# Optimization experiments

Measured on AMD Instinct MI355X. Metric: run time of the kernel, lower is better.

The kernel has to match this reference:

```python
import jax, jax.numpy as jnp
import numpy as np
import math

B, T, C = 4, 2048, 1024
N_HEADS = 16
D_HEAD = C // N_HEADS


def _rope_tables(d_head, max_seq_len):
    half = d_head // 2
    theta = 1.0 / (10000.0 ** (jnp.arange(half, dtype=jnp.float32) / half))
    pos = jnp.arange(max_seq_len, dtype=jnp.float32)
    freqs = jnp.outer(pos, theta)  # [S, half]
    cos = jnp.concatenate([jnp.cos(freqs), jnp.cos(freqs)], axis=-1)  # [S, d_head]
    sin = jnp.concatenate([jnp.sin(freqs), jnp.sin(freqs)], axis=-1)
    return cos, sin


def _rotate_half(x):
    d = x.shape[-1] // 2
    return jnp.concatenate([-x[..., d:], x[..., :d]], axis=-1)


def _apply_rope(x, cos, sin):
    # x: [B, H, T, d_head]; cos/sin: [T, d_head] broadcast over B,H
    return x * cos[None, None] + _rotate_half(x) * sin[None, None]


def setup_inputs() -> dict:
    key = jax.random.key(0)
    k1, k2, k3 = jax.random.split(key, 3)
    x = jax.random.normal(k1, (B, T, C), dtype=jnp.float32)
    W_qkv = jax.random.normal(k2, (C, 3 * C), dtype=jnp.float32) * (1.0 / math.sqrt(C))
    W_proj = jax.random.normal(k3, (C, C), dtype=jnp.float32) * (1.0 / math.sqrt(C))
    return {"x": x, "W_qkv": W_qkv, "W_proj": W_proj}


def reference(x, W_qkv, W_proj):
    b, t, c = x.shape
    qkv = x @ W_qkv  # [B, T, 3C]
    q, k, v = jnp.split(qkv, 3, axis=-1)

    def reshape(z):
        return z.reshape(b, t, N_HEADS, D_HEAD).transpose(0, 2, 1, 3)  # [B,H,T,dh]

    q, k, v = reshape(q), reshape(k), reshape(v)

    cos, sin = _rope_tables(D_HEAD, t)
    q = _apply_rope(q, cos, sin)
    k = _apply_rope(k, cos, sin)

    scale = 1.0 / math.sqrt(D_HEAD)
    att = jnp.einsum('bhqd,bhkd->bhqk', q, k) * scale  # [B,H,T,T]
    causal = jnp.tril(jnp.ones((t, t), dtype=bool))
    att = jnp.where(causal[None, None], att, -jnp.inf)
    att = jax.nn.softmax(att, axis=-1)
    out = jnp.einsum('bhqk,bhkd->bhqd', att, v)  # [B,H,T,dh]
    out = out.transpose(0, 2, 1, 3).reshape(b, t, c)
    return out @ W_proj
```

## Files before the change

kernel.cpp:

```cpp
#include <hip/hip_runtime.h>
#include <stdint.h>

#define Bz 4
#define Tz 2048
#define Cz 1024
#define NHz 16
#define DHz 64
#define Mz (Bz*Tz)

typedef unsigned short u16;
typedef __attribute__((ext_vector_type(8))) short short8;
typedef __attribute__((ext_vector_type(8))) unsigned short ushort8v;
typedef __attribute__((ext_vector_type(4))) unsigned short u16x4;
typedef __attribute__((ext_vector_type(4))) float f32x4;
typedef __attribute__((ext_vector_type(2))) unsigned int uint2v;

__device__ __forceinline__ float bf2f(u16 u){
  union { unsigned int i; float f; } v; v.i = ((unsigned int)u) << 16; return v.f;
}
__device__ __forceinline__ u16 f2bf(float f){
  union { float f; unsigned int i; } v; v.f = f;
  unsigned int r = v.i + 0x7FFFu + ((v.i >> 16) & 1u);
  return (u16)(r >> 16);
}


__global__ void k_cast_bf16(const float* __restrict__ in, u16* __restrict__ out, int n4){
  int i = blockIdx.x*256 + threadIdx.x;
  if (i >= n4) return;
  float4 v = ((const float4*)in)[i];
  u16x4 o;
  o[0] = f2bf(v.x); o[1] = f2bf(v.y); o[2] = f2bf(v.z); o[3] = f2bf(v.w);
  *(u16x4*)(out + (size_t)i*4) = o;
}

__global__ void k_transpose_cast(const float* __restrict__ W, u16* __restrict__ Wt, int K, int N){
  __shared__ float tile[32][33];
  int n0 = blockIdx.x*32, k0 = blockIdx.y*32;
  int tx = threadIdx.x, ty = threadIdx.y;
  #pragma unroll
  for (int i = 0; i < 32; i += 8)
    tile[ty+i][tx] = W[(size_t)(k0+ty+i)*N + n0 + tx];
  __syncthreads();
  #pragma unroll
  for (int i = 0; i < 32; i += 8)
    Wt[(size_t)(n0+ty+i)*K + k0 + tx] = f2bf(tile[tx][ty+i]);
}

__global__ void k_rope_tables(float* __restrict__ cosT, float* __restrict__ sinT){
  int idx = blockIdx.x*256 + threadIdx.x;
  int t = idx >> 5, i = idx & 31;
  float theta = exp2f(-(float)i * (13.287712379549449f / 32.0f));
  float ang = (float)t * theta;
  cosT[idx] = cosf(ang);
  sinT[idx] = sinf(ang);
}

#define GLDS(src, dstE) __builtin_amdgcn_global_load_lds( \
    (const __attribute__((address_space(1))) unsigned int*)(src), \
    (__attribute__((address_space(3))) unsigned int*)(lds + (dstE)), 16, 0, 0)

template<int Nn, int Kk, bool OUT_BF16, bool ROPE>
__global__ __launch_bounds__(512, 2) void k_gemm8(const u16* __restrict__ A, const u16* __restrict__ Bt,
                       void* __restrict__ Cout, u16* __restrict__ vTout,
                       const float* __restrict__ cosT, const float* __restrict__ sinT){
  extern __shared__ u16 lds[];
  constexpr int NT = Kk/64;
  constexpr int BUFE = 24576;
  constexpr int NWG = (Mz/128)*(Nn/256);
  const int wg = (blockIdx.x & 7)*(NWG/8) + (blockIdx.x >> 3);
  const int bm = wg & 63, bn = wg >> 6;
  const int tid = threadIdx.x, lane = tid & 63, w = tid >> 6;
  const int wm = w >> 2, wn = w & 3;
  const int g = lane >> 4, r = lane & 15;

  const int srow8 = lane >> 3;
  const int sslot = (lane & 7) ^ srow8;
  const u16* asrc = A  + (size_t)(bm*128 + w*16 + srow8)*Kk + sslot*8;
  const u16* bsrc = Bt + (size_t)(bn*256 + w*16 + srow8)*Kk + sslot*8;
  const int dA  = w*1024 + lane*8;
  const int dB0 = 8192 + w*1024 + lane*8;
  const int dB1 = 16384 + w*1024 + lane*8;

  int a_off[2][2][2], b_off[2][2][2];
  #pragma unroll
  for (int rq = 0; rq < 2; ++rq)
    #pragma unroll
    for (int fi = 0; fi < 2; ++fi)
      #pragma unroll
      for (int kc = 0; kc < 2; ++kc){
        int row = wm*64 + rq*32 + fi*16 + r;
        a_off[rq][fi][kc] = (row*128 + kc*64 + g*16) ^ ((r & 7) << 4);
        int rowb = wn*64 + rq*32 + fi*16 + r;
        b_off[rq][fi][kc] = 16384 + ((rowb*128 + kc*64 + g*16) ^ ((r & 7) << 4));
      }

  f32x4 acc[4][4] = {};

  {
    GLDS(asrc,                     dA);        GLDS(asrc + 8*(size_t)Kk,                     dA + 512);
    GLDS(bsrc,                     dB0);       GLDS(bsrc + 8*(size_t)Kk,                     dB0 + 512);
    GLDS(bsrc + 128*(size_t)Kk,    dB1);       GLDS(bsrc + 136*(size_t)Kk,                   dB1 + 512);
    GLDS(asrc + 64,                BUFE + dA); GLDS(asrc + 64 + 8*(size_t)Kk,                BUFE + dA + 512);
    GLDS(bsrc + 64,                BUFE + dB0);GLDS(bsrc + 64 + 8*(size_t)Kk,                BUFE + dB0 + 512);
    GLDS(bsrc + 64 + 128*(size_t)Kk, BUFE + dB1); GLDS(bsrc + 64 + 136*(size_t)Kk,           BUFE + dB1 + 512);
  }

  int bufc = 0;
  #pragma unroll 1
  for (int t = 0; t < NT; ++t){
    if (t + 1 < NT) asm volatile("s_waitcnt vmcnt(6)" ::: "memory");
    else            asm volatile("s_waitcnt vmcnt(0)" ::: "memory");
    __builtin_amdgcn_s_barrier();

    const int cbB = bufc*(BUFE*2);
    const bool pre = (t + 2 < NT);
    int bufn = bufc + 2; if (bufn >= 3) bufn -= 3;
    const int nE = bufn*BUFE;
    const size_t ko = (size_t)(t+2)*64;

    #define LD8(off) (*(const short8*)((const char*)lds + (off)))
    short8 af0k0, af0k1, af1k0, af1k1;
    short8 b0f0k0, b0f0k1, b0f1k0, b0f1k1;
    short8 b1f0k0, b1f0k1, b1f1k0, b1f1k1;

    af0k0 = LD8(cbB + a_off[0][0][0]); af0k1 = LD8(cbB + a_off[0][0][1]);
    af1k0 = LD8(cbB + a_off[0][1][0]); af1k1 = LD8(cbB + a_off[0][1][1]);
    b0f0k0 = LD8(cbB + b_off[0][0][0]); b0f0k1 = LD8(cbB + b_off[0][0][1]);
    b0f1k0 = LD8(cbB + b_off[0][1][0]); b0f1k1 = LD8(cbB + b_off[0][1][1]);
    if (pre){ GLDS(asrc + ko, nE + dA); GLDS(asrc + ko + 8*(size_t)Kk, nE + dA + 512); }
    __builtin_amdgcn_s_setprio(1);
    acc[0][0] = __builtin_amdgcn_mfma_f32_16x16x32_bf16(af0k0, b0f0k0, acc[0][0], 0,0,0);
    acc[0][0] = __builtin_amdgcn_mfma_f32_16x16x32_bf16(af0k1, b0f0k1, acc[0][0], 0,0,0);
    acc[0][1] = __builtin_amdgcn_mfma_f32_16x16x32_bf16(af0k0, b0f1k0, acc[0][1], 0,0,0);
    acc[0][1] = __builtin_amdgcn_mfma_f32_16x16x32_bf16(af0k1, b0f1k1, acc[0][1], 0,0,0);
    acc[1][0] = __builtin_amdgcn_mfma_f32_16x16x32_bf16(af1k0, b0f0k0, acc[1][0], 0,0,0);
    acc[1][0] = __builtin_amdgcn_mfma_f32_16x16x32_bf16(af1k1, b0f0k1, acc[1][0], 0,0,0);
    acc[1][1] = __builtin_amdgcn_mfma_f32_16x16x32_bf16(af1k0, b0f1k0, acc[1][1], 0,0,0);
    acc[1][1] = __builtin_amdgcn_mfma_f32_16x16x32_bf16(af1k1, b0f1k1, acc[1][1], 0,0,0);
    __builtin_amdgcn_s_setprio(0);

    b1f0k0 = LD8(cbB + b_off[1][0][0]); b1f0k1 = LD8(cbB + b_off[1][0][1]);
    b1f1k0 = LD8(cbB + b_off[1][1][0]); b1f1k1 = LD8(cbB + b_off[1][1][1]);
    if (pre){ GLDS(bsrc + ko, nE + dB0); GLDS(bsrc + ko + 8*(size_t)Kk, nE + dB0 + 512); }
    __builtin_amdgcn_s_setprio(1);
    acc[0][2] = __builtin_amdgcn_mfma_f32_16x16x32_bf16(af0k0, b1f0k0, acc[0][2], 0,0,0);
    acc[0][2] = __builtin_amdgcn_mfma_f32_16x16x32_bf16(af0k1, b1f0k1, acc[0][2], 0,0,0);
    acc[0][3] = __builtin_amdgcn_mfma_f32_16x16x32_bf16(af0k0, b1f1k0, acc[0][3], 0,0,0);
    acc[0][3] = __builtin_amdgcn_mfma_f32_16x16x32_bf16(af0k1, b1f1k1, acc[0][3], 0,0,0);
    acc[1][2] = __builtin_amdgcn_mfma_f32_16x16x32_bf16(af1k0, b1f0k0, acc[1][2], 0,0,0);
    acc[1][2] = __builtin_amdgcn_mfma_f32_16x16x32_bf16(af1k1, b1f0k1, acc[1][2], 0,0,0);
    acc[1][3] = __builtin_amdgcn_mfma_f32_16x16x32_bf16(af1k0, b1f1k0, acc[1][3], 0,0,0);
    acc[1][3] = __builtin_amdgcn_mfma_f32_16x16x32_bf16(af1k1, b1f1k1, acc[1][3], 0,0,0);
    __builtin_amdgcn_s_setprio(0);

    af0k0 = LD8(cbB + a_off[1][0][0]); af0k1 = LD8(cbB + a_off[1][0][1]);
    af1k0 = LD8(cbB + a_off[1][1][0]); af1k1 = LD8(cbB + a_off[1][1][1]);
    if (pre){ GLDS(bsrc + ko + 128*(size_t)Kk, nE + dB1); GLDS(bsrc + ko + 136*(size_t)Kk, nE + dB1 + 512); }
    __builtin_amdgcn_s_setprio(1);
    acc[2][2] = __builtin_amdgcn_mfma_f32_16x16x32_bf16(af0k0, b1f0k0, acc[2][2], 0,0,0);
    acc[2][2] = __builtin_amdgcn_mfma_f32_16x16x32_bf16(af0k1, b1f0k1, acc[2][2], 0,0,0);
    acc[2][3] = __builtin_amdgcn_mfma_f32_16x16x32_bf16(af0k0, b1f1k0, acc[2][3], 0,0,0);
    acc[2][3] = __builtin_amdgcn_mfma_f32_16x16x32_bf16(af0k1, b1f1k1, acc[2][3], 0,0,0);
    acc[3][2] = __builtin_amdgcn_mfma_f32_16x16x32_bf16(af1k0, b1f0k0, acc[3][2], 0,0,0);
    acc[3][2] = __builtin_amdgcn_mfma_f32_16x16x32_bf16(af1k1, b1f0k1, acc[3][2], 0,0,0);
    acc[3][3] = __builtin_amdgcn_mfma_f32_16x16x32_bf16(af1k0, b1f1k0, acc[3][3], 0,0,0);
    acc[3][3] = __builtin_amdgcn_mfma_f32_16x16x32_bf16(af1k1, b1f1k1, acc[3][3], 0,0,0);
    __builtin_amdgcn_s_setprio(0);

    __builtin_amdgcn_s_setprio(1);
    acc[2][0] = __builtin_amdgcn_mfma_f32_16x16x32_bf16(af0k0, b0f0k0, acc[2][0], 0,0,0);
    acc[2][0] = __builtin_amdgcn_mfma_f32_16x16x32_bf16(af0k1, b0f0k1, acc[2][0], 0,0,0);
    acc[2][1] = __builtin_amdgcn_mfma_f32_16x16x32_bf16(af0k0, b0f1k0, acc[2][1], 0,0,0);
    acc[2][1] = __builtin_amdgcn_mfma_f32_16x16x32_bf16(af0k1, b0f1k1, acc[2][1], 0,0,0);
    acc[3][0] = __builtin_amdgcn_mfma_f32_16x16x32_bf16(af1k0, b0f0k0, acc[3][0], 0,0,0);
    acc[3][0] = __builtin_amdgcn_mfma_f32_16x16x32_bf16(af1k1, b0f0k1, acc[3][0], 0,0,0);
    acc[3][1] = __builtin_amdgcn_mfma_f32_16x16x32_bf16(af1k0, b0f1k0, acc[3][1], 0,0,0);
    acc[3][1] = __builtin_amdgcn_mfma_f32_16x16x32_bf16(af1k1, b0f1k1, acc[3][1], 0,0,0);
    __builtin_amdgcn_s_setprio(0);
    #undef LD8

    ++bufc; if (bufc >= 3) bufc = 0;
  }

  const int nbase = bn*256 + wn*64;
  if (ROPE && nbase >= 2048){
    const int b = (bm*128) >> 11;
    const int h = (nbase >> 6) & 15;
    #pragma unroll
    for (int ri = 0; ri < 4; ++ri){
      const int m0 = bm*128 + wm*64 + ri*16 + 4*g;
      const int t0 = m0 & (Tz-1);
      #pragma unroll
      for (int cj = 0; cj < 4; ++cj){
        const int d = cj*16 + r;
        u16x4 o;
        #pragma unroll
        for (int jj = 0; jj < 4; ++jj) o[jj] = f2bf(acc[ri][cj][jj]);
        *(u16x4*)(vTout + ((size_t)((b*16 + h)*64 + d))*2048 + t0) = o;
      }
    }
  } else if (ROPE){
    const float qs = (nbase < 1024) ? 0.18033688011112042f : 1.0f;
    #pragma unroll
    for (int ri = 0; ri < 4; ++ri)
      #pragma unroll
      for (int jj = 0; jj < 4; ++jj){
        const int m = bm*128 + wm*64 + ri*16 + 4*g + jj;
        const int t = m & (Tz-1);
        #pragma unroll
        for (int cj = 0; cj < 2; ++cj){
          const int ch = cj*16 + r;
          float cv = cosT[t*32 + ch];
          float sv = sinT[t*32 + ch];
          float lo = acc[ri][cj][jj], hi = acc[ri][cj+2][jj];
          ((u16*)Cout)[(size_t)m*Nn + nbase + ch]      = f2bf((lo*cv - hi*sv)*qs);
          ((u16*)Cout)[(size_t)m*Nn + nbase + ch + 32] = f2bf((hi*cv + lo*sv)*qs);
        }
      }
  } else {
    #pragma unroll
    for (int ri = 0; ri < 4; ++ri)
      #pragma unroll
      for (int cj = 0; cj < 4; ++cj)
        #pragma unroll
        for (int jj = 0; jj < 4; ++jj){
          const size_t m = bm*128 + wm*64 + ri*16 + 4*g + jj;
          const size_t n = (size_t)nbase + cj*16 + r;
          if (OUT_BF16) ((u16*)Cout)[m*Nn + n] = f2bf(acc[ri][cj][jj]);
          else          ((float*)Cout)[m*Nn + n] = acc[ri][cj][jj];
        }
  }
}

__global__ __launch_bounds__(512) void k_attn2(const u16* __restrict__ qkv,
                                               const u16* __restrict__ vT,
                                               u16* __restrict__ att){
  __shared__ u16 K_lds[2*4096];
  __shared__ u16 V_lds[2*4096];
  __shared__ u16 P_lds[8*16*72];

  const int bh = blockIdx.x;
  const int b = bh >> 4, h = bh & 15;
  const int tid = threadIdx.x;
  const int w = tid >> 6;
  const int lane = tid & 63;
  const int g = lane >> 4;
  const int ql = lane & 15;
  u16* Pw = P_lds + w*16*72;

  const int srow  = lane >> 3;
  const int sslot = (lane & 7) ^ srow;
  const u16* ksrc = qkv + ((size_t)(b*Tz + 8*w + srow))*3072 + 1024 + h*64 + sslot*8;
  const u16* vsrc = vT  + ((size_t)bh*64 + 8*w + srow)*2048 + sslot*8;
  u16* kdst = K_lds + w*512 + lane*8;
  u16* vdst = V_lds + w*512 + lane*8;

  short8 ones;
  #pragma unroll
  for (int i = 0; i < 8; ++i) ones[i] = (short)0x3F80;

  int fofs[4][2];
  #pragma unroll
  for (int t = 0; t < 4; ++t){
    int row = 16*t + ql;
    fofs[t][0] = (row*128 + 16*g)      ^ ((row & 7) << 4);
    fofs[t][1] = (row*128 + 64 + 16*g) ^ ((row & 7) << 4);
  }

  #pragma unroll 1
  for (int half = 0; half < 2; ++half){
    const int qt = (half == 0) ? blockIdx.y : (15 - blockIdx.y);
    const int qr0w = qt*128 + w*16;
    const int nt = 2*qt + 2;

    const u16* qsrc = qkv + (size_t)(b*Tz + qr0w + ql)*3072 + h*64;
    short8 qf0 = *(const short8*)(qsrc + g*8);
    short8 qf1 = *(const short8*)(qsrc + 32 + g*8);

    f32x4 acc[4] = {{0,0,0,0},{0,0,0,0},{0,0,0,0},{0,0,0,0}};
    f32x4 accl = {0,0,0,0};

    __builtin_amdgcn_global_load_lds(
      (const __attribute__((address_space(1))) unsigned int*)(ksrc),
      (__attribute__((address_space(3))) unsigned int*)(kdst), 16, 0, 0);
    __builtin_amdgcn_global_load_lds(
      (const __attribute__((address_space(1))) unsigned int*)(vsrc),
      (__attribute__((address_space(3))) unsigned int*)(vdst), 16, 0, 0);
    __syncthreads();

    #pragma unroll 2
    for (int kt = 0; kt < nt; ++kt){
      const int buf = kt & 1;
      if (kt + 1 < nt){
        __builtin_amdgcn_global_load_lds(
          (const __attribute__((address_space(1))) unsigned int*)(ksrc + (size_t)(kt+1)*64*3072),
          (__attribute__((address_space(3))) unsigned int*)(kdst + (buf^1)*4096), 16, 0, 0);
        __builtin_amdgcn_global_load_lds(
          (const __attribute__((address_space(1))) unsigned int*)(vsrc + (kt+1)*64),
          (__attribute__((address_space(3))) unsigned int*)(vdst + (buf^1)*4096), 16, 0, 0);
      }
      const char* Kb = (const char*)(K_lds + buf*4096);
      const char* Vb = (const char*)(V_lds + buf*4096);
      const int kv0 = kt*64;

      f32x4 st[4];
      __builtin_amdgcn_s_setprio(1);
      #pragma unroll
      for (int t = 0; t < 4; ++t){
        short8 kf0 = *(const short8*)(Kb + fofs[t][0]);
        short8 kf1 = *(const short8*)(Kb + fofs[t][1]);
        f32x4 z = {0,0,0,0};
        z = __builtin_amdgcn_mfma_f32_16x16x32_bf16(kf0, qf0, z, 0, 0, 0);
        z = __builtin_amdgcn_mfma_f32_16x16x32_bf16(kf1, qf1, z, 0, 0, 0);
        st[t] = z;
      }
      __builtin_amdgcn_s_setprio(0);

      if (kv0 + 63 > qr0w){
        const int qg = qr0w + ql;
        #pragma unroll
        for (int t = 0; t < 4; ++t)
          #pragma unroll
          for (int j = 0; j < 4; ++j)
            if (kv0 + 16*t + 4*g + j > qg) st[t][j] = -1e30f;
      }

      #pragma unroll
      for (int t = 0; t < 4; ++t){
        float p0, p1, p2, p3;
        asm("v_exp_f32 %0, %1" : "=v"(p0) : "v"(st[t][0]));
        asm("v_exp_f32 %0, %1" : "=v"(p1) : "v"(st[t][1]));
        asm("v_exp_f32 %0, %1" : "=v"(p2) : "v"(st[t][2]));
        asm("v_exp_f32 %0, %1" : "=v"(p3) : "v"(st[t][3]));
        unsigned int lov, hiv;
        asm("v_cvt_pk_bf16_f32 %0, %1, %2" : "=v"(lov) : "v"(p0), "v"(p1));
        asm("v_cvt_pk_bf16_f32 %0, %1, %2" : "=v"(hiv) : "v"(p2), "v"(p3));
        uint2v pv; pv[0] = lov; pv[1] = hiv;
        *(uint2v*)((char*)Pw + ql*144 + (16*t + 4*g)*2) = pv;
      }

      short8 pf0 = *(const short8*)((char*)Pw + ql*144 + 16*g);
      short8 pf1 = *(const short8*)((char*)Pw + ql*144 + 64 + 16*g);
      __builtin_amdgcn_s_setprio(1);
      accl = __builtin_amdgcn_mfma_f32_16x16x32_bf16(pf0, ones, accl, 0, 0, 0);
      accl = __builtin_amdgcn_mfma_f32_16x16x32_bf16(pf1, ones, accl, 0, 0, 0);
      #pragma unroll
      for (int dt = 0; dt < 4; ++dt){
        short8 vf0 = *(const short8*)(Vb + fofs[dt][0]);
        short8 vf1 = *(const short8*)(Vb + fofs[dt][1]);
        acc[dt] = __builtin_amdgcn_mfma_f32_16x16x32_bf16(pf0, vf0, acc[dt], 0, 0, 0);
        acc[dt] = __builtin_amdgcn_mfma_f32_16x16x32_bf16(pf1, vf1, acc[dt], 0, 0, 0);
      }
      __builtin_amdgcn_s_setprio(0);
      __syncthreads();
    }

    float lj[4];
    #pragma unroll
    for (int j = 0; j < 4; ++j) lj[j] = 1.0f / accl[j];
    #pragma unroll
    for (int dt = 0; dt < 4; ++dt)
      #pragma unroll
      for (int j = 0; j < 4; ++j)
        att[(size_t)(b*Tz + qr0w + 4*g + j)*Cz + h*64 + dt*16 + ql] = f2bf(acc[dt][j]*lj[j]);
  }
}


extern "C" void kernel_launch(void* const* d_in, const int* in_sizes, int n_in,
                              void* d_out, int out_size, void* d_ws, size_t ws_size,
                              hipStream_t stream){
  const float* x     = (const float*)d_in[0];
  const float* Wqkv  = (const float*)d_in[1];
  const float* Wproj = (const float*)d_in[2];
  float* out = (float*)d_out;
  char* ws = (char*)d_ws;

  u16*  xb   = (u16*)(ws);
  u16*  wqt  = (u16*)(ws + 16777216);
  u16*  wpt  = (u16*)(ws + 23068672);
  u16*  qkv  = (u16*)(ws + 25165824);
  u16*  vTr  = (u16*)(ws + 75497472);
  float* cosT = (float*)(ws + 92274688);
  float* sinT = (float*)(ws + 92536832);

  hipFuncSetAttribute(reinterpret_cast<const void*>(k_gemm8<3072,1024,true,true>),
                      hipFuncAttributeMaxDynamicSharedMemorySize, 147456);
  hipFuncSetAttribute(reinterpret_cast<const void*>(k_gemm8<1024,1024,false,false>),
                      hipFuncAttributeMaxDynamicSharedMemorySize, 147456);

  k_cast_bf16<<<Mz*Cz/4/256, 256, 0, stream>>>(x, xb, Mz*Cz/4);
  k_transpose_cast<<<dim3(3072/32, 1024/32), dim3(32,8), 0, stream>>>(Wqkv, wqt, 1024, 3072);
  k_transpose_cast<<<dim3(1024/32, 1024/32), dim3(32,8), 0, stream>>>(Wproj, wpt, 1024, 1024);
  k_rope_tables<<<Tz*32/256, 256, 0, stream>>>(cosT, sinT);

  k_gemm8<3072, 1024, true, true><<<(Mz/128)*(3072/256), 512, 147456, stream>>>(
      xb, wqt, qkv, vTr, cosT, sinT);
  k_attn2<<<dim3(Bz*NHz, 8), 512, 0, stream>>>(qkv, vTr, xb);
  k_gemm8<1024, 1024, false, false><<<(Mz/128)*(1024/256), 512, 147456, stream>>>(
      xb, wpt, out, nullptr, nullptr, nullptr);
}
```

Measured before the change: 161.5 us.

## Restructure GEMM main loop into two barrier-synchronized phases with hoisted A fragments

Reorganizes the QKV GEMM inner loop into two phases. All A fragments and the first half of the B fragments are loaded up front, and 16 MFMAs run per phase, with the global-to-LDS prefetches split 3/3 across the phases. The vmcnt wait and barrier move from the top of the iteration to the end, with a prologue wait added before the loop. Extra s_barriers and explicit lgkmcnt(0) waits are inserted so the waves stay in lockstep, ping-pong style. The aim is better overlap of LDS reads, global prefetch and MFMA issue. The cost is more barriers per iteration and higher register pressure from holding all A fragments at once.

```diff
diff --git a/kernel.cpp b/kernel.cpp
--- a/kernel.cpp
+++ b/kernel.cpp
@@ -105,14 +105,12 @@
     GLDS(bsrc + 64,                BUFE + dB0);GLDS(bsrc + 64 + 8*(size_t)Kk,                BUFE + dB0 + 512);
     GLDS(bsrc + 64 + 128*(size_t)Kk, BUFE + dB1); GLDS(bsrc + 64 + 136*(size_t)Kk,           BUFE + dB1 + 512);
   }
+  asm volatile("s_waitcnt vmcnt(6)" ::: "memory");
+  __builtin_amdgcn_s_barrier();
 
   int bufc = 0;
   #pragma unroll 1
   for (int t = 0; t < NT; ++t){
-    if (t + 1 < NT) asm volatile("s_waitcnt vmcnt(6)" ::: "memory");
-    else            asm volatile("s_waitcnt vmcnt(0)" ::: "memory");
-    __builtin_amdgcn_s_barrier();
-
     const int cbB = bufc*(BUFE*2);
     const bool pre = (t + 2 < NT);
     int bufn = bufc + 2; if (bufn >= 3) bufn -= 3;
@@ -120,64 +118,70 @@
     const size_t ko = (size_t)(t+2)*64;
 
     #define LD8(off) (*(const short8*)((const char*)lds + (off)))
-    short8 af0k0, af0k1, af1k0, af1k1;
-    short8 b0f0k0, b0f0k1, b0f1k0, b0f1k1;
-    short8 b1f0k0, b1f0k1, b1f1k0, b1f1k1;
-
-    af0k0 = LD8(cbB + a_off[0][0][0]); af0k1 = LD8(cbB + a_off[0][0][1]);
-    af1k0 = LD8(cbB + a_off[0][1][0]); af1k1 = LD8(cbB + a_off[0][1][1]);
-    b0f0k0 = LD8(cbB + b_off[0][0][0]); b0f0k1 = LD8(cbB + b_off[0][0][1]);
-    b0f1k0 = LD8(cbB + b_off[0][1][0]); b0f1k1 = LD8(cbB + b_off[0][1][1]);
-    if (pre){ GLDS(asrc + ko, nE + dA); GLDS(asrc + ko + 8*(size_t)Kk, nE + dA + 512); }
+
+    short8 a0k0 = LD8(cbB + a_off[0][0][0]), a0k1 = LD8(cbB + a_off[0][0][1]);
+    short8 a1k0 = LD8(cbB + a_off[0][1][0]), a1k1 = LD8(cbB + a_off[0][1][1]);
+    short8 a2k0 = LD8(cbB + a_off[1][0][0]), a2k1 = LD8(cbB + a_off[1][0][1]);
+    short8 a3k0 = LD8(cbB + a_off[1][1][0]), a3k1 = LD8(cbB + a_off[1][1][1]);
+    short8 b0k0 = LD8(cbB + b_off[0][0][0]), b0k1 = LD8(cbB + b_off[0][0][1]);
+    short8 b1k0 = LD8(cbB + b_off[0][1][0]), b1k1 = LD8(cbB + b_off[0][1][1]);
+    if (pre){
+      GLDS(asrc + ko,                 nE + dA);
+      GLDS(asrc + ko + 8*(size_t)Kk,  nE + dA + 512);
+      GLDS(bsrc + ko,                 nE + dB0);
+    }
+    __builtin_amdgcn_s_barrier();
+    asm volatile("s_waitcnt lgkmcnt(0)" ::: "memory");
     __builtin_amdgcn_s_setprio(1);
-    acc[0][0] = __builtin_amdgcn_mfma_f32_16x16x32_bf16(af0k0, b0f0k0, acc[0][0], 0,0,0);
-    acc[0][0] = __builtin_amdgcn_mfma_f32_16x16x32_bf16(af0k1, b0f0k1, acc[0][0], 0,0,0);
-    acc[0][1] = __builtin_amdgcn_mfma_f32_16x16x32_bf16(af0k0, b0f1k0, acc[0][1], 0,0,0);
-    acc[0][1] = __builtin_amdgcn_mfma_f32_16x16x32_bf16(af0k1, b0f1k1, acc[0][1], 0,0,0);
-    acc[1][0] = __builtin_amdgcn_mfma_f32_16x16x32_bf16(af1k0, b0f0k0, acc[1][0], 0,0,0);
-    acc[1][0] = __builtin_amdgcn_mfma_f32_16x16x32_bf16(af1k1, b0f0k1, acc[1][0], 0,0,0);
-    acc[1][1] = __builtin_amdgcn_mfma_f32_16x16x32_bf16(af1k0, b0f1k0, acc[1][1], 0,0,0);
-    acc[1][1] = __builtin_amdgcn_mfma_f32_16x16x32_bf16(af1k1, b0f1k1, acc[1][1], 0,0,0);
+    acc[0][0] = __builtin_amdgcn_mfma_f32_16x16x32_bf16(a0k0, b0k0, acc[0][0], 0,0,0);
+    acc[0][0] = __builtin_amdgcn_mfma_f32_16x16x32_bf16(a0k1, b0k1, acc[0][0], 0,0,0);
+    acc[0][1] = __builtin_amdgcn_mfma_f32_16x16x32_bf16(a0k0, b1k0, acc[0][1], 0,0,0);
+    acc[0][1] = __builtin_amdgcn_mfma_f32_16x16x32_bf16(a0k1, b1k1, acc[0][1], 0,0,0);
+    acc[1][0] = __builtin_amdgcn_mfma_f32_16x16x32_bf16(a1k0, b0k0, acc[1][0], 0,0,0);
+    acc[1][0] = __builtin_amdgcn_mfma_f32_16x16x32_bf16(a1k1, b0k1, acc[1][0], 0,0,0);
+    acc[1][1] = __builtin_amdgcn_mfma_f32_16x16x32_bf16(a1k0, b1k0, acc[1][1], 0,0,0);
+    acc[1][1] = __builtin_amdgcn_mfma_f32_16x16x32_bf16(a1k1, b1k1, acc[1][1], 0,0,0);
+    acc[2][0] = __builtin_amdgcn_mfma_f32_16x16x32_bf16(a2k0, b0k0, acc[2][0], 0,0,0);
+    acc[2][0] = __builtin_amdgcn_mfma_f32_16x16x32_bf16(a2k1, b0k1, acc[2][0], 0,0,0);
+    acc[2][1] = __builtin_amdgcn_mfma_f32_16x16x32_bf16(a2k0, b1k0, acc[2][1], 0,0,0);
+    acc[2][1] = __builtin_amdgcn_mfma_f32_16x16x32_bf16(a2k1, b1k1, acc[2][1], 0,0,0);
+    acc[3][0] = __builtin_amdgcn_mfma_f32_16x16x32_bf16(a3k0, b0k0, acc[3][0], 0,0,0);
+    acc[3][0] = __builtin_amdgcn_mfma_f32_16x16x32_bf16(a3k1, b0k1, acc[3][0], 0,0,0);
+    acc[3][1] = __builtin_amdgcn_mfma_f32_16x16x32_bf16(a3k0, b1k0, acc[3][1], 0,0,0);
+    acc[3][1] = __builtin_amdgcn_mfma_f32_16x16x32_bf16(a3k1, b1k1, acc[3][1], 0,0,0);
     __builtin_amdgcn_s_setprio(0);
-
-    b1f0k0 = LD8(cbB + b_off[1][0][0]); b1f0k1 = LD8(cbB + b_off[1][0][1]);
-    b1f1k0 = LD8(cbB + b_off[1][1][0]); b1f1k1 = LD8(cbB + b_off[1][1][1]);
-    if (pre){ GLDS(bsrc + ko, nE + dB0); GLDS(bsrc + ko + 8*(size_t)Kk, nE + dB0 + 512); }
+    __builtin_amdgcn_s_barrier();
+
+    short8 c0k0 = LD8(cbB + b_off[1][0][0]), c0k1 = LD8(cbB + b_off[1][0][1]);
+    short8 c1k0 = LD8(cbB + b_off[1][1][0]), c1k1 = LD8(cbB + b_off[1][1][1]);
+    if (pre){
+      GLDS(bsrc + ko + 8*(size_t)Kk,   nE + dB0 + 512);
+      GLDS(bsrc + ko + 128*(size_t)Kk, nE + dB1);
+      GLDS(bsrc + ko + 136*(size_t)Kk, nE + dB1 + 512);
+    }
+    __builtin_amdgcn_s_barrier();
+    asm volatile("s_waitcnt lgkmcnt(0)" ::: "memory");
     __builtin_amdgcn_s_setprio(1);
-    acc[0][2] = __builtin_amdgcn_mfma_f32_16x16x32_bf16(af0k0, b1f0k0, acc[0][2], 0,0,0);
-    acc[0][2] = __builtin_amdgcn_mfma_f32_16x16x32_bf16(af0k1, b1f0k1, acc[0][2], 0,0,0);
-    acc[0][3] = __builtin_amdgcn_mfma_f32_16x16x32_bf16(af0k0, b1f1k0, acc[0][3], 0,0,0);
-    acc[0][3] = __builtin_amdgcn_mfma_f32_16x16x32_bf16(af0k1, b1f1k1, acc[0][3], 0,0,0);
-    acc[1][2] = __builtin_amdgcn_mfma_f32_16x16x32_bf16(af1k0, b1f0k0, acc[1][2], 0,0,0);
-    acc[1][2] = __builtin_amdgcn_mfma_f32_16x16x32_bf16(af1k1, b1f0k1, acc[1][2], 0,0,0);
-    acc[1][3] = __builtin_amdgcn_mfma_f32_16x16x32_bf16(af1k0, b1f1k0, acc[1][3], 0,0,0);
-    acc[1][3] = __builtin_amdgcn_mfma_f32_16x16x32_bf16(af1k1, b1f1k1, acc[1][3], 0,0,0);
+    acc[0][2] = __builtin_amdgcn_mfma_f32_16x16x32_bf16(a0k0, c0k0, acc[0][2], 0,0,0);
+    acc[0][2] = __builtin_amdgcn_mfma_f32_16x16x32_bf16(a0k1, c0k1, acc[0][2], 0,0,0);
+    acc[0][3] = __builtin_amdgcn_mfma_f32_16x16x32_bf16(a0k0, c1k0, acc[0][3], 0,0,0);
+    acc[0][3] = __builtin_amdgcn_mfma_f32_16x16x32_bf16(a0k1, c1k1, acc[0][3], 0,0,0);
+    acc[1][2] = __builtin_amdgcn_mfma_f32_16x16x32_bf16(a1k0, c0k0, acc[1][2], 0,0,0);
+    acc[1][2] = __builtin_amdgcn_mfma_f32_16x16x32_bf16(a1k1, c0k1, acc[1][2], 0,0,0);
+    acc[1][3] = __builtin_amdgcn_mfma_f32_16x16x32_bf16(a1k0, c1k0, acc[1][3], 0,0,0);
+    acc[1][3] = __builtin_amdgcn_mfma_f32_16x16x32_bf16(a1k1, c1k1, acc[1][3], 0,0,0);
+    acc[2][2] = __builtin_amdgcn_mfma_f32_16x16x32_bf16(a2k0, c0k0, acc[2][2], 0,0,0);
+    acc[2][2] = __builtin_amdgcn_mfma_f32_16x16x32_bf16(a2k1, c0k1, acc[2][2], 0,0,0);
+    acc[2][3] = __builtin_amdgcn_mfma_f32_16x16x32_bf16(a2k0, c1k0, acc[2][3], 0,0,0);
+    acc[2][3] = __builtin_amdgcn_mfma_f32_16x16x32_bf16(a2k1, c1k1, acc[2][3], 0,0,0);
+    acc[3][2] = __builtin_amdgcn_mfma_f32_16x16x32_bf16(a3k0, c0k0, acc[3][2], 0,0,0);
+    acc[3][2] = __builtin_amdgcn_mfma_f32_16x16x32_bf16(a3k1, c0k1, acc[3][2], 0,0,0);
+    acc[3][3] = __builtin_amdgcn_mfma_f32_16x16x32_bf16(a3k0, c1k0, acc[3][3], 0,0,0);
+    acc[3][3] = __builtin_amdgcn_mfma_f32_16x16x32_bf16(a3k1, c1k1, acc[3][3], 0,0,0);
     __builtin_amdgcn_s_setprio(0);
-
-    af0k0 = LD8(cbB + a_off[1][0][0]); af0k1 = LD8(cbB + a_off[1][0][1]);
-    af1k0 = LD8(cbB + a_off[1][1][0]); af1k1 = LD8(cbB + a_off[1][1][1]);
-    if (pre){ GLDS(bsrc + ko + 128*(size_t)Kk, nE + dB1); GLDS(bsrc + ko + 136*(size_t)Kk, nE + dB1 + 512); }
-    __builtin_amdgcn_s_setprio(1);
-    acc[2][2] = __builtin_amdgcn_mfma_f32_16x16x32_bf16(af0k0, b1f0k0, acc[2][2], 0,0,0);
-    acc[2][2] = __builtin_amdgcn_mfma_f32_16x16x32_bf16(af0k1, b1f0k1, acc[2][2], 0,0,0);
-    acc[2][3] = __builtin_amdgcn_mfma_f32_16x16x32_bf16(af0k0, b1f1k0, acc[2][3], 0,0,0);
-    acc[2][3] = __builtin_amdgcn_mfma_f32_16x16x32_bf16(af0k1, b1f1k1, acc[2][3], 0,0,0);
-    acc[3][2] = __builtin_amdgcn_mfma_f32_16x16x32_bf16(af1k0, b1f0k0, acc[3][2], 0,0,0);
-    acc[3][2] = __builtin_amdgcn_mfma_f32_16x16x32_bf16(af1k1, b1f0k1, acc[3][2], 0,0,0);
-    acc[3][3] = __builtin_amdgcn_mfma_f32_16x16x32_bf16(af1k0, b1f1k0, acc[3][3], 0,0,0);
-    acc[3][3] = __builtin_amdgcn_mfma_f32_16x16x32_bf16(af1k1, b1f1k1, acc[3][3], 0,0,0);
-    __builtin_amdgcn_s_setprio(0);
-
-    __builtin_amdgcn_s_setprio(1);
-    acc[2][0] = __builtin_amdgcn_mfma_f32_16x16x32_bf16(af0k0, b0f0k0, acc[2][0], 0,0,0);
-    acc[2][0] = __builtin_amdgcn_mfma_f32_16x16x32_bf16(af0k1, b0f0k1, acc[2][0], 0,0,0);
-    acc[2][1] = __builtin_amdgcn_mfma_f32_16x16x32_bf16(af0k0, b0f1k0, acc[2][1], 0,0,0);
-    acc[2][1] = __builtin_amdgcn_mfma_f32_16x16x32_bf16(af0k1, b0f1k1, acc[2][1], 0,0,0);
-    acc[3][0] = __builtin_amdgcn_mfma_f32_16x16x32_bf16(af1k0, b0f0k0, acc[3][0], 0,0,0);
-    acc[3][0] = __builtin_amdgcn_mfma_f32_16x16x32_bf16(af1k1, b0f0k1, acc[3][0], 0,0,0);
-    acc[3][1] = __builtin_amdgcn_mfma_f32_16x16x32_bf16(af1k0, b0f1k0, acc[3][1], 0,0,0);
-    acc[3][1] = __builtin_amdgcn_mfma_f32_16x16x32_bf16(af1k1, b0f1k1, acc[3][1], 0,0,0);
-    __builtin_amdgcn_s_setprio(0);
+    if (t + 2 < NT)      asm volatile("s_waitcnt vmcnt(6)" ::: "memory");
+    else if (t + 1 < NT) asm volatile("s_waitcnt vmcnt(0)" ::: "memory");
+    __builtin_amdgcn_s_barrier();
     #undef LD8
 
     ++bufc; if (bufc >= 3) bufc = 0;
```

New measurement: 165.5 us. +2.5%, slower.

## Replace QKV GEMM with simple single-buffered 128x128 tile kernel

Applied to the files above, without the earlier changes.

The QKV projection moves from the 8-wave, triple-buffered 128x256 tile kernel to a new 256-thread kernel with 128x128 tiles, K-step 32, and a single LDS buffer with syncs around each step. The RoPE and V-transpose epilogue is carried over unchanged, and the ROPE path is removed from k_gemm8. The smaller tile doubles the workgroup count and uses far less LDS, which may raise occupancy. In exchange it drops the prefetch pipelining, so global-to-LDS latency is exposed on every K step.

```diff
diff --git a/kernel.cpp b/kernel.cpp
--- a/kernel.cpp
+++ b/kernel.cpp
@@ -56,14 +56,117 @@
   sinT[idx] = sinf(ang);
 }
 
+template<int Nn, int Kk, bool ROPE>
+__global__ void k_gemm128(const u16* __restrict__ A, const u16* __restrict__ Bt,
+                          void* __restrict__ Cout, u16* __restrict__ vTout,
+                          const float* __restrict__ cosT, const float* __restrict__ sinT){
+  __shared__ u16 Asub[128*32];
+  __shared__ u16 Bsub[128*32];
+  constexpr int NWG = (Mz/128)*(Nn/128);
+  const int wg = (blockIdx.x & 7)*(NWG/8) + (blockIdx.x >> 3);
+  const int bm = wg & 63, bn = wg >> 6;
+  const int tid = threadIdx.x, lane = tid & 63, w = tid >> 6;
+  const int g = lane >> 4, r = lane & 15;
+  const int wm = (w >> 1)*64, wn = (w & 1)*64;
+  f32x4 acc[4][4] = {};
+
+  const int srow4 = lane >> 2;
+  const int sslot = (lane & 3) ^ (srow4 & 3);
+  const u16* arow = A  + (size_t)(bm*128)*Kk;
+  const u16* brow = Bt + (size_t)(bn*128)*Kk;
+
+  int a_ofs[4], b_ofs[4];
+  #pragma unroll
+  for (int i = 0; i < 4; ++i){
+    a_ofs[i] = (wm + i*16 + r)*64 + (((g ^ (r & 3)) & 3) << 4);
+    b_ofs[i] = (wn + i*16 + r)*64 + (((g ^ (r & 3)) & 3) << 4);
+  }
+
+  for (int k0 = 0; k0 < Kk; k0 += 32){
+    #pragma unroll
+    for (int ic = 0; ic < 2; ++ic){
+      int ch = w*2 + ic;
+      int row = ch*16 + srow4;
+      __builtin_amdgcn_global_load_lds(
+        (const __attribute__((address_space(1))) unsigned int*)(arow + (size_t)row*Kk + k0 + sslot*8),
+        (__attribute__((address_space(3))) unsigned int*)(Asub + ch*512 + lane*8), 16, 0, 0);
+      __builtin_amdgcn_global_load_lds(
+        (const __attribute__((address_space(1))) unsigned int*)(brow + (size_t)row*Kk + k0 + sslot*8),
+        (__attribute__((address_space(3))) unsigned int*)(Bsub + ch*512 + lane*8), 16, 0, 0);
+    }
+    __syncthreads();
+    short8 af[4], bfr[4];
+    #pragma unroll
+    for (int i = 0; i < 4; ++i){
+      af[i]  = *(const short8*)((const char*)Asub + a_ofs[i]);
+      bfr[i] = *(const short8*)((const char*)Bsub + b_ofs[i]);
+    }
+    __builtin_amdgcn_s_setprio(1);
+    #pragma unroll
+    for (int i = 0; i < 4; ++i)
+      #pragma unroll
+      for (int j = 0; j < 4; ++j)
+        acc[i][j] = __builtin_amdgcn_mfma_f32_16x16x32_bf16(af[i], bfr[j], acc[i][j], 0, 0, 0);
+    __builtin_amdgcn_s_setprio(0);
+    __syncthreads();
+  }
+
+  const int nbase = bn*128 + wn;
+  if (ROPE && nbase >= 2048){
+    const int b = bm >> 4;
+    const int h = (nbase >> 6) & 15;
+    #pragma unroll
+    for (int ri = 0; ri < 4; ++ri){
+      const int m0 = bm*128 + wm + ri*16 + 4*g;
+      const int t0 = m0 & (Tz-1);
+      #pragma unroll
+      for (int cj = 0; cj < 4; ++cj){
+        const int d = cj*16 + r;
+        u16x4 o;
+        #pragma unroll
+        for (int jj = 0; jj < 4; ++jj) o[jj] = f2bf(acc[ri][cj][jj]);
+        *(u16x4*)(vTout + ((size_t)((b*16 + h)*64 + d))*2048 + t0) = o;
+      }
+    }
+  } else if (ROPE){
+    const float qs = (nbase < 1024) ? 0.18033688011112042f : 1.0f;
+    #pragma unroll
+    for (int ri = 0; ri < 4; ++ri)
+      #pragma unroll
+      for (int jj = 0; jj < 4; ++jj){
+        const int m = bm*128 + wm + ri*16 + 4*g + jj;
+        const int t = m & (Tz-1);
+        #pragma unroll
+        for (int cj = 0; cj < 2; ++cj){
+          const int ch = cj*16 + r;
+          float cv = cosT[t*32 + ch];
+          float sv = sinT[t*32 + ch];
+          float lo = acc[ri][cj][jj], hi = acc[ri][cj+2][jj];
+          ((u16*)Cout)[(size_t)m*Nn + nbase + ch]      = f2bf((lo*cv - hi*sv)*qs);
+          ((u16*)Cout)[(size_t)m*Nn + nbase + ch + 32] = f2bf((hi*cv + lo*sv)*qs);
+        }
+      }
+  } else {
+    #pragma unroll
+    for (int ri = 0; ri < 4; ++ri)
+      #pragma unroll
+      for (int cj = 0; cj < 4; ++cj)
+        #pragma unroll
+        for (int jj = 0; jj < 4; ++jj){
+          const size_t m = bm*128 + wm + ri*16 + 4*g + jj;
+          const size_t n = (size_t)nbase + cj*16 + r;
+          ((float*)Cout)[m*Nn + n] = acc[ri][cj][jj];
+        }
+  }
+}
+
 #define GLDS(src, dstE) __builtin_amdgcn_global_load_lds( \
     (const __attribute__((address_space(1))) unsigned int*)(src), \
     (__attribute__((address_space(3))) unsigned int*)(lds + (dstE)), 16, 0, 0)
 
-template<int Nn, int Kk, bool OUT_BF16, bool ROPE>
+template<int Nn, int Kk, bool OUT_BF16>
 __global__ __launch_bounds__(512, 2) void k_gemm8(const u16* __restrict__ A, const u16* __restrict__ Bt,
-                       void* __restrict__ Cout, u16* __restrict__ vTout,
-                       const float* __restrict__ cosT, const float* __restrict__ sinT){
+                       void* __restrict__ Cout){
   extern __shared__ u16 lds[];
   constexpr int NT = Kk/64;
   constexpr int BUFE = 24576;
@@ -184,53 +287,17 @@
   }
 
   const int nbase = bn*256 + wn*64;
-  if (ROPE && nbase >= 2048){
-    const int b = (bm*128) >> 11;
-    const int h = (nbase >> 6) & 15;
-    #pragma unroll
-    for (int ri = 0; ri < 4; ++ri){
-      const int m0 = bm*128 + wm*64 + ri*16 + 4*g;
-      const int t0 = m0 & (Tz-1);
-      #pragma unroll
-      for (int cj = 0; cj < 4; ++cj){
-        const int d = cj*16 + r;
-        u16x4 o;
-        #pragma unroll
-        for (int jj = 0; jj < 4; ++jj) o[jj] = f2bf(acc[ri][cj][jj]);
-        *(u16x4*)(vTout + ((size_t)((b*16 + h)*64 + d))*2048 + t0) = o;
-      }
-    }
-  } else if (ROPE){
-    const float qs = (nbase < 1024) ? 0.18033688011112042f : 1.0f;
-    #pragma unroll
-    for (int ri = 0; ri < 4; ++ri)
+  #pragma unroll
+  for (int ri = 0; ri < 4; ++ri)
+    #pragma unroll
+    for (int cj = 0; cj < 4; ++cj)
       #pragma unroll
       for (int jj = 0; jj < 4; ++jj){
-        const int m = bm*128 + wm*64 + ri*16 + 4*g + jj;
-        const int t = m & (Tz-1);
-        #pragma unroll
-        for (int cj = 0; cj < 2; ++cj){
-          const int ch = cj*16 + r;
-          float cv = cosT[t*32 + ch];
-          float sv = sinT[t*32 + ch];
-          float lo = acc[ri][cj][jj], hi = acc[ri][cj+2][jj];
-          ((u16*)Cout)[(size_t)m*Nn + nbase + ch]      = f2bf((lo*cv - hi*sv)*qs);
-          ((u16*)Cout)[(size_t)m*Nn + nbase + ch + 32] = f2bf((hi*cv + lo*sv)*qs);
-        }
-      }
-  } else {
-    #pragma unroll
-    for (int ri = 0; ri < 4; ++ri)
-      #pragma unroll
-      for (int cj = 0; cj < 4; ++cj)
-        #pragma unroll
-        for (int jj = 0; jj < 4; ++jj){
-          const size_t m = bm*128 + wm*64 + ri*16 + 4*g + jj;
-          const size_t n = (size_t)nbase + cj*16 + r;
-          if (OUT_BF16) ((u16*)Cout)[m*Nn + n] = f2bf(acc[ri][cj][jj]);
-          else          ((float*)Cout)[m*Nn + n] = acc[ri][cj][jj];
-        }
-  }
+        const size_t m = bm*128 + wm*64 + ri*16 + 4*g + jj;
+        const size_t n = (size_t)nbase + cj*16 + r;
+        if (OUT_BF16) ((u16*)Cout)[m*Nn + n] = f2bf(acc[ri][cj][jj]);
+        else          ((float*)Cout)[m*Nn + n] = acc[ri][cj][jj];
+      }
 }
 
 __global__ __launch_bounds__(512) void k_attn2(const u16* __restrict__ qkv,
@@ -385,9 +452,7 @@
   float* cosT = (float*)(ws + 92274688);
   float* sinT = (float*)(ws + 92536832);
 
-  hipFuncSetAttribute(reinterpret_cast<const void*>(k_gemm8<3072,1024,true,true>),
-                      hipFuncAttributeMaxDynamicSharedMemorySize, 147456);
-  hipFuncSetAttribute(reinterpret_cast<const void*>(k_gemm8<1024,1024,false,false>),
+  hipFuncSetAttribute(reinterpret_cast<const void*>(k_gemm8<1024,1024,false>),
                       hipFuncAttributeMaxDynamicSharedMemorySize, 147456);
 
   k_cast_bf16<<<Mz*Cz/4/256, 256, 0, stream>>>(x, xb, Mz*Cz/4);
@@ -395,9 +460,9 @@
   k_transpose_cast<<<dim3(1024/32, 1024/32), dim3(32,8), 0, stream>>>(Wproj, wpt, 1024, 1024);
   k_rope_tables<<<Tz*32/256, 256, 0, stream>>>(cosT, sinT);
 
-  k_gemm8<3072, 1024, true, true><<<(Mz/128)*(3072/256), 512, 147456, stream>>>(
+  k_gemm128<3072, 1024, true><<<(Mz/128)*(3072/128), 256, 0, stream>>>(
       xb, wqt, qkv, vTr, cosT, sinT);
   k_attn2<<<dim3(Bz*NHz, 8), 512, 0, stream>>>(qkv, vTr, xb);
-  k_gemm8<1024, 1024, false, false><<<(Mz/128)*(1024/256), 512, 147456, stream>>>(
-      xb, wpt, out, nullptr, nullptr, nullptr);
-}
+  k_gemm8<1024, 1024, false><<<(Mz/128)*(1024/256), 512, 147456, stream>>>(
+      xb, wpt, out);
+}
```

New measurement: 175.9 us. +8.9%, slower.

## Replace triple-buffered 128x256 GEMM with double-buffered 128x128 four-wave kernel

Applied to the files above, without the earlier changes.

Both GEMMs move from a 512-thread, 128x256-tile kernel with a three-stage LDS ring, interleaved prefetch and XCD-aware block swizzle to a 256-thread, 128x128-tile kernel with a two-stage double buffer in static shared memory and a plain 2D grid. Each wave still owns a 64x64 output tile, but all fragments are loaded up front and the next stage is issued at the top of the iteration. The smaller tile and LDS footprint allow more resident blocks per CU. The cost is lower reuse of each loaded tile, a full vmcnt(0) wait and barrier every iteration, and loss of the L2-friendly block remapping.

```diff
diff --git a/kernel.cpp b/kernel.cpp
--- a/kernel.cpp
+++ b/kernel.cpp
@@ -58,138 +58,93 @@
 
 #define GLDS(src, dstE) __builtin_amdgcn_global_load_lds( \
     (const __attribute__((address_space(1))) unsigned int*)(src), \
-    (__attribute__((address_space(3))) unsigned int*)(lds + (dstE)), 16, 0, 0)
-
-template<int Nn, int Kk, bool OUT_BF16, bool ROPE>
-__global__ __launch_bounds__(512, 2) void k_gemm8(const u16* __restrict__ A, const u16* __restrict__ Bt,
-                       void* __restrict__ Cout, u16* __restrict__ vTout,
-                       const float* __restrict__ cosT, const float* __restrict__ sinT){
-  extern __shared__ u16 lds[];
+    (__attribute__((address_space(3))) unsigned int*)((u16*)lds + (dstE)), 16, 0, 0)
+
+template<int Nn, int Kk, bool ROPE>
+__global__ __launch_bounds__(256, 4) void k_gemmdb(const u16* __restrict__ A, const u16* __restrict__ Bt,
+                        void* __restrict__ Cout, u16* __restrict__ vTout,
+                        const float* __restrict__ cosT, const float* __restrict__ sinT){
+  __shared__ u16 lds[2][16384];
   constexpr int NT = Kk/64;
-  constexpr int BUFE = 24576;
-  constexpr int NWG = (Mz/128)*(Nn/256);
-  const int wg = (blockIdx.x & 7)*(NWG/8) + (blockIdx.x >> 3);
-  const int bm = wg & 63, bn = wg >> 6;
+  const int bm = blockIdx.x, bn = blockIdx.y;
   const int tid = threadIdx.x, lane = tid & 63, w = tid >> 6;
-  const int wm = w >> 2, wn = w & 3;
+  const int wm = (w >> 1)*64, wn = (w & 1)*64;
   const int g = lane >> 4, r = lane & 15;
 
   const int srow8 = lane >> 3;
   const int sslot = (lane & 7) ^ srow8;
-  const u16* asrc = A  + (size_t)(bm*128 + w*16 + srow8)*Kk + sslot*8;
-  const u16* bsrc = Bt + (size_t)(bn*256 + w*16 + srow8)*Kk + sslot*8;
-  const int dA  = w*1024 + lane*8;
-  const int dB0 = 8192 + w*1024 + lane*8;
-  const int dB1 = 16384 + w*1024 + lane*8;
-
-  int a_off[2][2][2], b_off[2][2][2];
-  #pragma unroll
-  for (int rq = 0; rq < 2; ++rq)
-    #pragma unroll
-    for (int fi = 0; fi < 2; ++fi)
-      #pragma unroll
-      for (int kc = 0; kc < 2; ++kc){
-        int row = wm*64 + rq*32 + fi*16 + r;
-        a_off[rq][fi][kc] = (row*128 + kc*64 + g*16) ^ ((r & 7) << 4);
-        int rowb = wn*64 + rq*32 + fi*16 + r;
-        b_off[rq][fi][kc] = 16384 + ((rowb*128 + kc*64 + g*16) ^ ((r & 7) << 4));
-      }
+  const u16* asrc = A  + (size_t)(bm*128 + w*32 + srow8)*Kk + sslot*8;
+  const u16* bsrc = Bt + (size_t)(bn*128 + w*32 + srow8)*Kk + sslot*8;
+  const int dA = w*2048 + lane*8;
+  const int dB = 8192 + w*2048 + lane*8;
+
+  int a_off[4][2], b_off[4][2];
+  #pragma unroll
+  for (int i = 0; i < 4; ++i)
+    #pragma unroll
+    for (int kc = 0; kc < 2; ++kc){
+      int row = wm + i*16 + r;
+      a_off[i][kc] = (row*128 + kc*64 + g*16) ^ ((r & 7) << 4);
+      int rowb = wn + i*16 + r;
+      b_off[i][kc] = 16384 + ((rowb*128 + kc*64 + g*16) ^ ((r & 7) << 4));
+    }
 
   f32x4 acc[4][4] = {};
 
-  {
-    GLDS(asrc,                     dA);        GLDS(asrc + 8*(size_t)Kk,                     dA + 512);
-    GLDS(bsrc,                     dB0);       GLDS(bsrc + 8*(size_t)Kk,                     dB0 + 512);
-    GLDS(bsrc + 128*(size_t)Kk,    dB1);       GLDS(bsrc + 136*(size_t)Kk,                   dB1 + 512);
-    GLDS(asrc + 64,                BUFE + dA); GLDS(asrc + 64 + 8*(size_t)Kk,                BUFE + dA + 512);
-    GLDS(bsrc + 64,                BUFE + dB0);GLDS(bsrc + 64 + 8*(size_t)Kk,                BUFE + dB0 + 512);
-    GLDS(bsrc + 64 + 128*(size_t)Kk, BUFE + dB1); GLDS(bsrc + 64 + 136*(size_t)Kk,           BUFE + dB1 + 512);
-  }
-
-  int bufc = 0;
+#define STG(t, bi) do{ \
+    const size_t ko_ = (size_t)(t)*64; \
+    const int be_ = (bi)*16384; \
+    GLDS(asrc + ko_,                 be_ + dA);        \
+    GLDS(asrc + ko_ +  8*(size_t)Kk, be_ + dA + 512);  \
+    GLDS(asrc + ko_ + 16*(size_t)Kk, be_ + dA + 1024); \
+    GLDS(asrc + ko_ + 24*(size_t)Kk, be_ + dA + 1536); \
+    GLDS(bsrc + ko_,                 be_ + dB);        \
+    GLDS(bsrc + ko_ +  8*(size_t)Kk, be_ + dB + 512);  \
+    GLDS(bsrc + ko_ + 16*(size_t)Kk, be_ + dB + 1024); \
+    GLDS(bsrc + ko_ + 24*(size_t)Kk, be_ + dB + 1536); \
+  }while(0)
+
+  STG(0, 0);
+  asm volatile("s_waitcnt vmcnt(0)" ::: "memory");
+  __builtin_amdgcn_s_barrier();
+
+  int buf = 0;
   #pragma unroll 1
   for (int t = 0; t < NT; ++t){
-    if (t + 1 < NT) asm volatile("s_waitcnt vmcnt(6)" ::: "memory");
-    else            asm volatile("s_waitcnt vmcnt(0)" ::: "memory");
-    __builtin_amdgcn_s_barrier();
-
-    const int cbB = bufc*(BUFE*2);
-    const bool pre = (t + 2 < NT);
-    int bufn = bufc + 2; if (bufn >= 3) bufn -= 3;
-    const int nE = bufn*BUFE;
-    const size_t ko = (size_t)(t+2)*64;
-
-    #define LD8(off) (*(const short8*)((const char*)lds + (off)))
-    short8 af0k0, af0k1, af1k0, af1k1;
-    short8 b0f0k0, b0f0k1, b0f1k0, b0f1k1;
-    short8 b1f0k0, b1f0k1, b1f1k0, b1f1k1;
-
-    af0k0 = LD8(cbB + a_off[0][0][0]); af0k1 = LD8(cbB + a_off[0][0][1]);
-    af1k0 = LD8(cbB + a_off[0][1][0]); af1k1 = LD8(cbB + a_off[0][1][1]);
-    b0f0k0 = LD8(cbB + b_off[0][0][0]); b0f0k1 = LD8(cbB + b_off[0][0][1]);
-    b0f1k0 = LD8(cbB + b_off[0][1][0]); b0f1k1 = LD8(cbB + b_off[0][1][1]);
-    if (pre){ GLDS(asrc + ko, nE + dA); GLDS(asrc + ko + 8*(size_t)Kk, nE + dA + 512); }
+    if (t + 1 < NT) STG(t+1, buf^1);
+    const char* Lb = (const char*)lds + buf*32768;
+    short8 af[4][2], bf[4][2];
+    #pragma unroll
+    for (int i = 0; i < 4; ++i)
+      #pragma unroll
+      for (int kc = 0; kc < 2; ++kc){
+        af[i][kc] = *(const short8*)(Lb + a_off[i][kc]);
+        bf[i][kc] = *(const short8*)(Lb + b_off[i][kc]);
+      }
     __builtin_amdgcn_s_setprio(1);
-    acc[0][0] = __builtin_amdgcn_mfma_f32_16x16x32_bf16(af0k0, b0f0k0, acc[0][0], 0,0,0);
-    acc[0][0] = __builtin_amdgcn_mfma_f32_16x16x32_bf16(af0k1, b0f0k1, acc[0][0], 0,0,0);
-    acc[0][1] = __builtin_amdgcn_mfma_f32_16x16x32_bf16(af0k0, b0f1k0, acc[0][1], 0,0,0);
-    acc[0][1] = __builtin_amdgcn_mfma_f32_16x16x32_bf16(af0k1, b0f1k1, acc[0][1], 0,0,0);
-    acc[1][0] = __builtin_amdgcn_mfma_f32_16x16x32_bf16(af1k0, b0f0k0, acc[1][0], 0,0,0);
-    acc[1][0] = __builtin_amdgcn_mfma_f32_16x16x32_bf16(af1k1, b0f0k1, acc[1][0], 0,0,0);
-    acc[1][1] = __builtin_amdgcn_mfma_f32_16x16x32_bf16(af1k0, b0f1k0, acc[1][1], 0,0,0);
-    acc[1][1] = __builtin_amdgcn_mfma_f32_16x16x32_bf16(af1k1, b0f1k1, acc[1][1], 0,0,0);
+    #pragma unroll
+    for (int i = 0; i < 4; ++i)
+      #pragma unroll
+      for (int j = 0; j < 4; ++j){
+        acc[i][j] = __builtin_amdgcn_mfma_f32_16x16x32_bf16(af[i][0], bf[j][0], acc[i][j], 0,0,0);
+        acc[i][j] = __builtin_amdgcn_mfma_f32_16x16x32_bf16(af[i][1], bf[j][1], acc[i][j], 0,0,0);
+      }
     __builtin_amdgcn_s_setprio(0);
-
-    b1f0k0 = LD8(cbB + b_off[1][0][0]); b1f0k1 = LD8(cbB + b_off[1][0][1]);
-    b1f1k0 = LD8(cbB + b_off[1][1][0]); b1f1k1 = LD8(cbB + b_off[1][1][1]);
-    if (pre){ GLDS(bsrc + ko, nE + dB0); GLDS(bsrc + ko + 8*(size_t)Kk, nE + dB0 + 512); }
-    __builtin_amdgcn_s_setprio(1);
-    acc[0][2] = __builtin_amdgcn_mfma_f32_16x16x32_bf16(af0k0, b1f0k0, acc[0][2], 0,0,0);
-    acc[0][2] = __builtin_amdgcn_mfma_f32_16x16x32_bf16(af0k1, b1f0k1, acc[0][2], 0,0,0);
-    acc[0][3] = __builtin_amdgcn_mfma_f32_16x16x32_bf16(af0k0, b1f1k0, acc[0][3], 0,0,0);
-    acc[0][3] = __builtin_amdgcn_mfma_f32_16x16x32_bf16(af0k1, b1f1k1, acc[0][3], 0,0,0);
-    acc[1][2] = __builtin_amdgcn_mfma_f32_16x16x32_bf16(af1k0, b1f0k0, acc[1][2], 0,0,0);
-    acc[1][2] = __builtin_amdgcn_mfma_f32_16x16x32_bf16(af1k1, b1f0k1, acc[1][2], 0,0,0);
-    acc[1][3] = __builtin_amdgcn_mfma_f32_16x16x32_bf16(af1k0, b1f1k0, acc[1][3], 0,0,0);
-    acc[1][3] = __builtin_amdgcn_mfma_f32_16x16x32_bf16(af1k1, b1f1k1, acc[1][3], 0,0,0);
-    __builtin_amdgcn_s_setprio(0);
-
-    af0k0 = LD8(cbB + a_off[1][0][0]); af0k1 = LD8(cbB + a_off[1][0][1]);
-    af1k0 = LD8(cbB + a_off[1][1][0]); af1k1 = LD8(cbB + a_off[1][1][1]);
-    if (pre){ GLDS(bsrc + ko + 128*(size_t)Kk, nE + dB1); GLDS(bsrc + ko + 136*(size_t)Kk, nE + dB1 + 512); }
-    __builtin_amdgcn_s_setprio(1);
-    acc[2][2] = __builtin_amdgcn_mfma_f32_16x16x32_bf16(af0k0, b1f0k0, acc[2][2], 0,0,0);
-    acc[2][2] = __builtin_amdgcn_mfma_f32_16x16x32_bf16(af0k1, b1f0k1, acc[2][2], 0,0,0);
-    acc[2][3] = __builtin_amdgcn_mfma_f32_16x16x32_bf16(af0k0, b1f1k0, acc[2][3], 0,0,0);
-    acc[2][3] = __builtin_amdgcn_mfma_f32_16x16x32_bf16(af0k1, b1f1k1, acc[2][3], 0,0,0);
-    acc[3][2] = __builtin_amdgcn_mfma_f32_16x16x32_bf16(af1k0, b1f0k0, acc[3][2], 0,0,0);
-    acc[3][2] = __builtin_amdgcn_mfma_f32_16x16x32_bf16(af1k1, b1f0k1, acc[3][2], 0,0,0);
-    acc[3][3] = __builtin_amdgcn_mfma_f32_16x16x32_bf16(af1k0, b1f1k0, acc[3][3], 0,0,0);
-    acc[3][3] = __builtin_amdgcn_mfma_f32_16x16x32_bf16(af1k1, b1f1k1, acc[3][3], 0,0,0);
-    __builtin_amdgcn_s_setprio(0);
-
-    __builtin_amdgcn_s_setprio(1);
-    acc[2][0] = __builtin_amdgcn_mfma_f32_16x16x32_bf16(af0k0, b0f0k0, acc[2][0], 0,0,0);
-    acc[2][0] = __builtin_amdgcn_mfma_f32_16x16x32_bf16(af0k1, b0f0k1, acc[2][0], 0,0,0);
-    acc[2][1] = __builtin_amdgcn_mfma_f32_16x16x32_bf16(af0k0, b0f1k0, acc[2][1], 0,0,0);
-    acc[2][1] = __builtin_amdgcn_mfma_f32_16x16x32_bf16(af0k1, b0f1k1, acc[2][1], 0,0,0);
-    acc[3][0] = __builtin_amdgcn_mfma_f32_16x16x32_bf16(af1k0, b0f0k0, acc[3][0], 0,0,0);
-    acc[3][0] = __builtin_amdgcn_mfma_f32_16x16x32_bf16(af1k1, b0f0k1, acc[3][0], 0,0,0);
-    acc[3][1] = __builtin_amdgcn_mfma_f32_16x16x32_bf16(af1k0, b0f1k0, acc[3][1], 0,0,0);
-    acc[3][1] = __builtin_amdgcn_mfma_f32_16x16x32_bf16(af1k1, b0f1k1, acc[3][1], 0,0,0);
-    __builtin_amdgcn_s_setprio(0);
-    #undef LD8
-
-    ++bufc; if (bufc >= 3) bufc = 0;
+    if (t + 1 < NT){
+      asm volatile("s_waitcnt vmcnt(0)" ::: "memory");
+      __builtin_amdgcn_s_barrier();
+      buf ^= 1;
+    }
   }
-
-  const int nbase = bn*256 + wn*64;
+#undef STG
+
+  const int nbase = bn*128 + wn;
   if (ROPE && nbase >= 2048){
-    const int b = (bm*128) >> 11;
+    const int b = bm >> 4;
     const int h = (nbase >> 6) & 15;
     #pragma unroll
     for (int ri = 0; ri < 4; ++ri){
-      const int m0 = bm*128 + wm*64 + ri*16 + 4*g;
+      const int m0 = bm*128 + wm + ri*16 + 4*g;
       const int t0 = m0 & (Tz-1);
       #pragma unroll
       for (int cj = 0; cj < 4; ++cj){
@@ -206,7 +161,7 @@
     for (int ri = 0; ri < 4; ++ri)
       #pragma unroll
       for (int jj = 0; jj < 4; ++jj){
-        const int m = bm*128 + wm*64 + ri*16 + 4*g + jj;
+        const int m = bm*128 + wm + ri*16 + 4*g + jj;
         const int t = m & (Tz-1);
         #pragma unroll
         for (int cj = 0; cj < 2; ++cj){
@@ -225,10 +180,9 @@
       for (int cj = 0; cj < 4; ++cj)
         #pragma unroll
         for (int jj = 0; jj < 4; ++jj){
-          const size_t m = bm*128 + wm*64 + ri*16 + 4*g + jj;
+          const size_t m = bm*128 + wm + ri*16 + 4*g + jj;
           const size_t n = (size_t)nbase + cj*16 + r;
-          if (OUT_BF16) ((u16*)Cout)[m*Nn + n] = f2bf(acc[ri][cj][jj]);
-          else          ((float*)Cout)[m*Nn + n] = acc[ri][cj][jj];
+          ((float*)Cout)[m*Nn + n] = acc[ri][cj][jj];
         }
   }
 }
@@ -385,19 +339,14 @@
   float* cosT = (float*)(ws + 92274688);
   float* sinT = (float*)(ws + 92536832);
 
-  hipFuncSetAttribute(reinterpret_cast<const void*>(k_gemm8<3072,1024,true,true>),
-                      hipFuncAttributeMaxDynamicSharedMemorySize, 147456);
-  hipFuncSetAttribute(reinterpret_cast<const void*>(k_gemm8<1024,1024,false,false>),
-                      hipFuncAttributeMaxDynamicSharedMemorySize, 147456);
-
   k_cast_bf16<<<Mz*Cz/4/256, 256, 0, stream>>>(x, xb, Mz*Cz/4);
   k_transpose_cast<<<dim3(3072/32, 1024/32), dim3(32,8), 0, stream>>>(Wqkv, wqt, 1024, 3072);
   k_transpose_cast<<<dim3(1024/32, 1024/32), dim3(32,8), 0, stream>>>(Wproj, wpt, 1024, 1024);
   k_rope_tables<<<Tz*32/256, 256, 0, stream>>>(cosT, sinT);
 
-  k_gemm8<3072, 1024, true, true><<<(Mz/128)*(3072/256), 512, 147456, stream>>>(
+  k_gemmdb<3072, 1024, true><<<dim3(Mz/128, 3072/128), 256, 0, stream>>>(
       xb, wqt, qkv, vTr, cosT, sinT);
   k_attn2<<<dim3(Bz*NHz, 8), 512, 0, stream>>>(qkv, vTr, xb);
-  k_gemm8<1024, 1024, false, false><<<(Mz/128)*(1024/256), 512, 147456, stream>>>(
+  k_gemmdb<1024, 1024, false><<<dim3(Mz/128, 1024/128), 256, 0, stream>>>(
       xb, wpt, out, nullptr, nullptr, nullptr);
 }
```

New measurement: 157.9 us. 1.02x faster.
